# Optimization experiments

Hardware: AMD Instinct MI355X
Metric: run time of the kernel (lower is better)

Reference implementation:

```python
import jax, jax.numpy as jnp
import numpy as np

V, E, H = 32000, 512, 1024  # vocab, embed_dim, hidden_dim
B, S = 32, 64
PAD = 0


def _init(key, shape, fan_in):
    return jax.random.normal(key, shape, jnp.float32) * (1.0 / np.sqrt(fan_in))


def setup_inputs() -> dict:
    key = jax.random.key(0)
    ks = jax.random.split(key, 16)
    tok_embed = _init(ks[0], (V, E), E).at[PAD].set(0.0)  # padding_idx row zeroed
    inp = {
        "image_emb": jax.random.normal(ks[1], (B, E), jnp.float32),
        "retrieved_emb": jax.random.normal(ks[2], (B, E), jnp.float32),
        "tokens_in": jax.random.randint(ks[3], (B, S), 0, V, jnp.int64),
        "tok_embed": tok_embed,
        "init_h_W": _init(ks[4], (H, E), E),
        "init_h_b": jnp.zeros((H,), jnp.float32),
        "gru_W_ih": _init(ks[5], (3 * H, 2 * E), 2 * E),
        "gru_W_hh": _init(ks[6], (3 * H, H), H),
        "gru_b_ih": jnp.zeros((3 * H,), jnp.float32),
        "gru_b_hh": jnp.zeros((3 * H,), jnp.float32),
        "gate_W": _init(ks[7], (1, H + 2 * E), H + 2 * E),
        "gate_b": jnp.zeros((1,), jnp.float32),
        "out_W": _init(ks[8], (V, H), H),
        "out_b": jnp.zeros((V,), jnp.float32),
    }
    return inp


def _gru_cell(x, h, W_ih, W_hh, b_ih, b_hh):
    # PyTorch GRU cell math
    gi = x @ W_ih.T + b_ih  # [B, 3H]
    gh = h @ W_hh.T + b_hh
    i_r, i_z, i_n = jnp.split(gi, 3, axis=-1)
    h_r, h_z, h_n = jnp.split(gh, 3, axis=-1)
    r = jax.nn.sigmoid(i_r + h_r)
    z = jax.nn.sigmoid(i_z + h_z)
    n = jnp.tanh(i_n + r * h_n)
    return (1.0 - z) * n + z * h


def reference(image_emb, retrieved_emb, tokens_in, tok_embed, init_h_W, init_h_b,
              gru_W_ih, gru_W_hh, gru_b_ih, gru_b_hh, gate_W, gate_b, out_W, out_b):
    tok = tok_embed[tokens_in]  # [B, S, E]
    h0 = jnp.tanh(image_emb @ init_h_W.T + init_h_b)  # [B, H]

    def step(h, x_t):
        gate_in = jnp.concatenate([h, image_emb, retrieved_emb], axis=-1)  # [B, H+2E]
        alpha = jax.nn.sigmoid(gate_in @ gate_W.T + gate_b)  # [B, 1]
        fused = alpha * image_emb + (1.0 - alpha) * retrieved_emb  # [B, E]
        gru_in = jnp.concatenate([x_t, fused], axis=-1)  # [B, 2E]
        h_new = _gru_cell(gru_in, h, gru_W_ih, gru_W_hh, gru_b_ih, gru_b_hh)
        logit = h_new @ out_W.T + out_b  # [B, V]
        return h_new, logit

    _, logits = jax.lax.scan(step, h0, jnp.swapaxes(tok, 0, 1))  # [S, B, V]
    return jnp.swapaxes(logits, 0, 1)  # [B, S, V]
```

## Files before the change

### kernel.cpp

```cpp
#include <hip/hip_runtime.h>
#include <hip/hip_bf16.h>
#include <stdint.h>

#define B_ 32
#define S_ 64
#define E_ 512
#define H_ 1024
#define V_ 32000
#define H3_ 3072
#define NPROD 64
#define NCONS 192
#define NGRID (NPROD + NCONS)
#define NPANEL 250
#define NBATCH 16
#define NJOBS (NPANEL * NBATCH)

typedef __bf16 bf16x8 __attribute__((ext_vector_type(8)));
typedef float f32x4 __attribute__((ext_vector_type(4)));
typedef unsigned long long u64_t;
using bf16 = __hip_bfloat16;

__device__ __forceinline__ unsigned short f2bf(float f) {
  __hip_bfloat16 h = __float2bfloat16(f);
  return __builtin_bit_cast(unsigned short, h);
}

__device__ __forceinline__ void async16(void* lds, const void* g) {
  __builtin_amdgcn_global_load_lds(
      (const __attribute__((address_space(1))) unsigned int*)g,
      (__attribute__((address_space(3))) unsigned int*)lds, 16, 0, 0);
}

__device__ __forceinline__ void st_u32(unsigned* p, unsigned v) {
  __hip_atomic_store(p, v, __ATOMIC_RELAXED, __HIP_MEMORY_SCOPE_AGENT);
}
__device__ __forceinline__ unsigned ld_u32(const unsigned* p) {
  return __hip_atomic_load(p, __ATOMIC_RELAXED, __HIP_MEMORY_SCOPE_AGENT);
}
__device__ __forceinline__ f32x4 ld16_mall(const void* p) {
  f32x4 r;
  asm volatile("global_load_dwordx4 %0, %1, off sc0 sc1" : "=v"(r) : "v"(p));
  return r;
}

__device__ __forceinline__ int hswz(int b, int ig) {
  return ((((b >> 4) * 32 + (ig >> 5)) * 64) + ((b & 15) + (((ig >> 3) & 3) << 4))) * 8 + (ig & 7);
}


__global__ void cvt_wb(const float* __restrict__ W, ushort* __restrict__ Wb, long n4) {
  long stride = (long)gridDim.x * blockDim.x;
  for (long i = (long)blockIdx.x * blockDim.x + threadIdx.x; i < n4; i += stride) {
    f32x4 v = *(const f32x4*)(W + i * 4);
    ushort4 o;
    o.x = f2bf(v[0]); o.y = f2bf(v[1]); o.z = f2bf(v[2]); o.w = f2bf(v[3]);
    ((ushort4*)Wb)[i] = o;
  }
}

__global__ void cvt_whh(const float* __restrict__ W, bf16* __restrict__ hi,
                        bf16* __restrict__ lo) {
  size_t idx = ((size_t)blockIdx.x * 256 + threadIdx.x) * 4;
  f32x4 v = *(const f32x4*)(W + idx);
#pragma unroll
  for (int j = 0; j < 4; ++j) {
    bf16 h = __float2bfloat16(v[j]);
    hi[idx + j] = h;
    lo[idx + j] = __float2bfloat16(v[j] - __bfloat162float(h));
  }
}

__global__ void gather_tok(const int* __restrict__ toks, const float* __restrict__ emb,
                           bf16* __restrict__ Abf) {
  int m = blockIdx.x;
  int b = m & 31, t = m >> 5;
  int token = toks[b * S_ + t];
  const float* src = emb + (size_t)token * E_;
  bf16* dst = Abf + (size_t)m * E_;
  int k = threadIdx.x * 4;
  f32x4 v = *(const f32x4*)(src + k);
  dst[k + 0] = __float2bfloat16(v[0]);
  dst[k + 1] = __float2bfloat16(v[1]);
  dst[k + 2] = __float2bfloat16(v[2]);
  dst[k + 3] = __float2bfloat16(v[3]);
}

__global__ void cvt_wihx(const float* __restrict__ Wih, bf16* __restrict__ Wx) {
  int j = blockIdx.x;
  int k = threadIdx.x * 4;
  f32x4 v = *(const f32x4*)(Wih + (size_t)j * 1024 + k);
  bf16* d = Wx + (size_t)j * 512 + k;
  d[0] = __float2bfloat16(v[0]);
  d[1] = __float2bfloat16(v[1]);
  d[2] = __float2bfloat16(v[2]);
  d[3] = __float2bfloat16(v[3]);
}

__global__ void h0_kernel(const float* __restrict__ img, const float* __restrict__ W,
                          const float* __restrict__ bias, float* __restrict__ h32,
                          bf16* __restrict__ hbf0) {
  __shared__ float sim[B_][E_ + 1];
  int tid = threadIdx.x;
  for (int i = tid; i < B_ * E_ / 4; i += 256) {
    f32x4 v = ((const f32x4*)img)[i];
    int r = (i * 4) / E_, c = (i * 4) % E_;
    sim[r][c + 0] = v[0]; sim[r][c + 1] = v[1]; sim[r][c + 2] = v[2]; sim[r][c + 3] = v[3];
  }
  __syncthreads();
  int b = tid & 31, il = tid >> 5;
  int i = blockIdx.x * 8 + il;
  const float* wr = W + (size_t)i * E_;
  float acc = 0.f;
  for (int k = 0; k < E_; k += 4) {
    f32x4 w4 = *(const f32x4*)(wr + k);
    acc += w4[0] * sim[b][k] + w4[1] * sim[b][k + 1] + w4[2] * sim[b][k + 2] + w4[3] * sim[b][k + 3];
  }
  float hv = tanhf(acc + bias[i]);
  h32[b * H_ + i] = hv;
  hbf0[hswz(b, i)] = __float2bfloat16(hv);
}

__global__ void uv_kernel(const float* __restrict__ img, const float* __restrict__ retr,
                          const float* __restrict__ Wih, float* __restrict__ u,
                          float* __restrict__ v) {
  int blk = blockIdx.x;
  bool isU = blk < 384;
  const float* src = isU ? img : retr;
  float* dst = isU ? u : v;
  int j0 = (isU ? blk : blk - 384) * 8;
  __shared__ float sim[B_][E_ + 1];
  int tid = threadIdx.x;
  for (int i = tid; i < B_ * E_ / 4; i += 256) {
    f32x4 vv = ((const f32x4*)src)[i];
    int r = (i * 4) / E_, c = (i * 4) % E_;
    sim[r][c + 0] = vv[0]; sim[r][c + 1] = vv[1]; sim[r][c + 2] = vv[2]; sim[r][c + 3] = vv[3];
  }
  __syncthreads();
  int b = tid & 31;
  int j = j0 + (tid >> 5);
  const float* wr = Wih + (size_t)j * 1024 + 512;
  float acc = 0.f;
  for (int k = 0; k < E_; k += 4) {
    f32x4 w4 = *(const f32x4*)(wr + k);
    acc += w4[0] * sim[b][k] + w4[1] * sim[b][k + 1] + w4[2] * sim[b][k + 2] + w4[3] * sim[b][k + 3];
  }
  dst[b * H3_ + j] = acc;
}

__global__ void cgate_kernel(const float* __restrict__ img, const float* __restrict__ retr,
                             const float* __restrict__ gW, const float* __restrict__ gb,
                             float* __restrict__ cg) {
  int b = blockIdx.x, tid = threadIdx.x;
  float acc = 0.f;
  for (int k = tid; k < E_; k += 256)
    acc += img[b * E_ + k] * gW[1024 + k] + retr[b * E_ + k] * gW[1536 + k];
  __shared__ float red[256];
  red[tid] = acc;
  __syncthreads();
  for (int s = 128; s > 0; s >>= 1) {
    if (tid < s) red[tid] += red[tid + s];
    __syncthreads();
  }
  if (tid == 0) cg[b] = red[0] + gb[0];
}

__device__ __forceinline__ void step_sync(unsigned* flags, int bi, unsigned val) {
  __syncthreads();
  if (threadIdx.x == 0) st_u32(flags + bi * 32, val);
  if (threadIdx.x < NPROD) {
    const unsigned* f = flags + threadIdx.x * 32;
    while (ld_u32(f) < val) __builtin_amdgcn_s_sleep(1);
  }
  __syncthreads();
}

__global__ __launch_bounds__(256, 1) void fused_persist(
    const bf16* __restrict__ WhhHi, const bf16* __restrict__ WhhLo,
    const float* __restrict__ gixAll, const float* __restrict__ u,
    const float* __restrict__ v, const float* __restrict__ cg,
    const float* __restrict__ gW, const float* __restrict__ bih,
    const float* __restrict__ bhh, const float* __restrict__ h32init,
    bf16* __restrict__ hbf, unsigned* __restrict__ flags,
    const bf16* __restrict__ Wb, const float* __restrict__ outb,
    float* __restrict__ out) {
  __shared__ __align__(16) char smem[32768];
  int bi = blockIdx.x;
  int tid = threadIdx.x;

  if (bi < NPROD) {
    int w = tid >> 6, l = tid & 63;
    int lr = l & 15, lk8 = (l >> 4) * 8;
    int kbase = w * 256;
    float(*red)[4][2][64][4] = (float(*)[4][2][64][4])smem;

    bf16x8 whi[3][8], wlo[3][8];
#pragma unroll
    for (int g = 0; g < 3; ++g)
#pragma unroll
      for (int ks = 0; ks < 8; ++ks) {
        size_t off = (size_t)(g * H_ + bi * 16 + lr) * H_ + kbase + ks * 32 + lk8;
        whi[g][ks] = *(const bf16x8*)(WhhHi + off);
        wlo[g][ks] = *(const bf16x8*)(WhhLo + off);
      }
    bf16x8 gwf[8];
#pragma unroll
    for (int ks = 0; ks < 8; ++ks) {
      int kk = (w * 8 + ks) * 32 + (l >> 4) * 8;
      f32x4 g0 = *(const f32x4*)(gW + kk);
      f32x4 g1 = *(const f32x4*)(gW + kk + 4);
      bf16x8 gf;
#pragma unroll
      for (int j = 0; j < 4; ++j) {
        gf[j] = __builtin_bit_cast(__bf16, f2bf(g0[j]));
        gf[j + 4] = __builtin_bit_cast(__bf16, f2bf(g1[j]));
      }
      gwf[ks] = gf;
    }

    int bq = tid >> 3;
    int il0 = (tid & 7) * 2;
    float uq[2][3], vq[2][3], biq[2][3], bhq[2][3], hold[2];
    float cgq = cg[bq];
#pragma unroll
    for (int q = 0; q < 2; ++q) {
      int ig = bi * 16 + il0 + q;
#pragma unroll
      for (int g = 0; g < 3; ++g) {
        uq[q][g] = u[bq * H3_ + g * H_ + ig];
        vq[q][g] = v[bq * H3_ + g * H_ + ig];
        biq[q][g] = bih[g * H_ + ig];
        bhq[q][g] = bhh[g * H_ + ig];
      }
      hold[q] = h32init[bq * H_ + ig];
    }
    int btq = bq >> 4, breg = bq & 3, lrow = ((bq & 15) >> 2) * 16;

    for (int t = 0; t < S_; ++t) {
      const char* hb = (const char*)hbf + (size_t)t * 65536;
      bf16x8 hh_all[2][8];
#pragma unroll
      for (int bt = 0; bt < 2; ++bt)
#pragma unroll
        for (int ks = 0; ks < 8; ++ks) {
          int off = ((bt * 32 + w * 8 + ks) * 64 + l) * 16;
          hh_all[bt][ks] = __builtin_bit_cast(bf16x8, ld16_mall(hb + off));
        }
      float gxv[2][3];
      {
        const float* gx = gixAll + ((size_t)t * B_ + bq) * H3_;
#pragma unroll
        for (int q = 0; q < 2; ++q) {
          int ig = bi * 16 + il0 + q;
          gxv[q][0] = gx[ig];
          gxv[q][1] = gx[H_ + ig];
          gxv[q][2] = gx[2 * H_ + ig];
        }
      }
      asm volatile("s_waitcnt vmcnt(0)" ::: "memory");
      __builtin_amdgcn_sched_barrier(0);

      f32x4 acc[4][2] = {};
#pragma unroll
      for (int ks = 0; ks < 8; ++ks) {
#pragma unroll
        for (int bt = 0; bt < 2; ++bt) {
          bf16x8 hh = hh_all[bt][ks];
          acc[0][bt] = __builtin_amdgcn_mfma_f32_16x16x32_bf16(hh, whi[0][ks], acc[0][bt], 0, 0, 0);
          acc[0][bt] = __builtin_amdgcn_mfma_f32_16x16x32_bf16(hh, wlo[0][ks], acc[0][bt], 0, 0, 0);
          acc[1][bt] = __builtin_amdgcn_mfma_f32_16x16x32_bf16(hh, whi[1][ks], acc[1][bt], 0, 0, 0);
          acc[1][bt] = __builtin_amdgcn_mfma_f32_16x16x32_bf16(hh, wlo[1][ks], acc[1][bt], 0, 0, 0);
          acc[2][bt] = __builtin_amdgcn_mfma_f32_16x16x32_bf16(hh, whi[2][ks], acc[2][bt], 0, 0, 0);
          acc[2][bt] = __builtin_amdgcn_mfma_f32_16x16x32_bf16(hh, wlo[2][ks], acc[2][bt], 0, 0, 0);
          acc[3][bt] = __builtin_amdgcn_mfma_f32_16x16x32_bf16(hh, gwf[ks], acc[3][bt], 0, 0, 0);
        }
      }
#pragma unroll
      for (int g = 0; g < 4; ++g)
#pragma unroll
        for (int bt = 0; bt < 2; ++bt)
          *(f32x4*)&red[w][g][bt][l][0] = acc[g][bt];
      __syncthreads();

      int lane0 = lrow + il0;
      float ad = red[0][3][btq][lane0][breg] + red[1][3][btq][lane0][breg] +
                 red[2][3][btq][lane0][breg] + red[3][3][btq][lane0][breg];
      float a = 1.f / (1.f + expf(-(ad + cgq)));
      unsigned short h16[2];
#pragma unroll
      for (int q = 0; q < 2; ++q) {
        int lane = lrow + il0 + q;
        float sr = red[0][0][btq][lane][breg] + red[1][0][btq][lane][breg] +
                   red[2][0][btq][lane][breg] + red[3][0][btq][lane][breg];
        float sz = red[0][1][btq][lane][breg] + red[1][1][btq][lane][breg] +
                   red[2][1][btq][lane][breg] + red[3][1][btq][lane][breg];
        float sn = red[0][2][btq][lane][breg] + red[1][2][btq][lane][breg] +
                   red[2][2][btq][lane][breg] + red[3][2][btq][lane][breg];
        float ir = gxv[q][0] + a * uq[q][0] + (1.f - a) * vq[q][0] + biq[q][0];
        float iz = gxv[q][1] + a * uq[q][1] + (1.f - a) * vq[q][1] + biq[q][1];
        float in_ = gxv[q][2] + a * uq[q][2] + (1.f - a) * vq[q][2] + biq[q][2];
        float r = 1.f / (1.f + expf(-(ir + sr + bhq[q][0])));
        float z = 1.f / (1.f + expf(-(iz + sz + bhq[q][1])));
        float nn = tanhf(in_ + r * (sn + bhq[q][2]));
        float hv = (1.f - z) * nn + z * hold[q];
        hold[q] = hv;
        h16[q] = f2bf(hv);
      }
      {
        unsigned hipack = (unsigned)h16[0] | ((unsigned)h16[1] << 16);
        int off = hswz(bq, bi * 16 + il0);
        unsigned* hi32 = (unsigned*)hbf + (size_t)(t + 1) * 16384;
        st_u32(hi32 + (off >> 1), hipack);
      }
      if (t < S_ - 1) step_sync(flags, bi, t + 1);
    }
    __syncthreads();
    if (tid == 0) st_u32(flags + bi * 32, S_);

  } else {
    int c = bi - NPROD;
    int l = tid & 63, w = tid >> 6;
    int wm = (w >> 1) * 64, wn = (w & 1) * 64;
    int lr = l & 15, lk = (l >> 4) * 8;
    bf16* Bld = (bf16*)smem;
    char* lB0 = smem + w * 1024;
    const char* hb_base = (const char*)hbf;

    for (int j = c; j < NJOBS; j += NCONS) {
      int batch = j / NPANEL;
      int panel = j - batch * NPANEL;
      int s0 = batch * 4 + 1;
      unsigned need = (unsigned)(batch * 4 + 4);
      if (w == 0) {
        const unsigned* f = flags + l * 32;
        while (ld_u32(f) < need) __builtin_amdgcn_s_sleep(16);
      }
      __builtin_amdgcn_sched_barrier(0);
      __builtin_amdgcn_s_barrier();
      __builtin_amdgcn_sched_barrier(0);

      const bf16* gb = Wb + (size_t)(panel * 128 + w * 16 + (l >> 2)) * 1024 + (l & 3) * 8;
      f32x4 acc[4][4] = {};
      bf16x8 afr[2][4];
#pragma unroll
      for (int mi = 0; mi < 4; ++mi) {
        int r16 = (wm >> 4) + mi;
        const char* p = hb_base + (size_t)(s0 + (r16 >> 1)) * 65536 +
                        (((r16 & 1) * 32 + 0) * 64 + l) * 16;
        afr[0][mi] = __builtin_bit_cast(bf16x8, ld16_mall(p));
      }
#pragma unroll
      for (int kt = 0; kt < 32; ++kt) {
        char* lB = lB0 + (kt & 1) * 8192;
        async16(lB, gb);
        async16(lB + 4096, gb + (size_t)64 * 1024);
        gb += 32;
        if (kt < 31) {
#pragma unroll
          for (int mi = 0; mi < 4; ++mi) {
            int r16 = (wm >> 4) + mi;
            const char* p = hb_base + (size_t)(s0 + (r16 >> 1)) * 65536 +
                            (((r16 & 1) * 32 + (kt + 1)) * 64 + l) * 16;
            afr[(kt + 1) & 1][mi] = __builtin_bit_cast(bf16x8, ld16_mall(p));
          }
          asm volatile("s_waitcnt vmcnt(4)" ::: "memory");
        } else {
          asm volatile("s_waitcnt vmcnt(0)" ::: "memory");
        }
        __builtin_amdgcn_sched_barrier(0);
        __builtin_amdgcn_s_barrier();
        __builtin_amdgcn_sched_barrier(0);
        const bf16* Bh = Bld + (kt & 1) * 4096;
        bf16x8 bfv[4];
#pragma unroll
        for (int ni = 0; ni < 4; ++ni)
          bfv[ni] = *(const bf16x8*)&Bh[(wn + ni * 16 + lr) * 32 + lk];
#pragma unroll
        for (int mi = 0; mi < 4; ++mi)
#pragma unroll
          for (int ni = 0; ni < 4; ++ni)
            acc[mi][ni] = __builtin_amdgcn_mfma_f32_16x16x32_bf16(afr[kt & 1][mi], bfv[ni],
                                                                  acc[mi][ni], 0, 0, 0);
      }
      int cr = (l >> 4) * 4, cc = l & 15;
#pragma unroll
      for (int mi = 0; mi < 4; ++mi)
#pragma unroll
        for (int ni = 0; ni < 4; ++ni) {
          int col = panel * 128 + wn + ni * 16 + cc;
          float bv = outb[col];
#pragma unroll
          for (int rr = 0; rr < 4; ++rr) {
            int gr = wm + mi * 16 + cr + rr;
            int t = s0 - 1 + (gr >> 5);
            int b = gr & 31;
            out[(size_t)(b * S_ + t) * V_ + col] = acc[mi][ni][rr] + bv;
          }
        }
    }
  }
}

__global__ __launch_bounds__(256) void gemm_bt(const bf16* __restrict__ A,
                                               const bf16* __restrict__ Bt,
                                               const float* __restrict__ bias,
                                               float* __restrict__ C, int M, int N, int K) {
  __shared__ bf16 Ald[128 * 32];
  __shared__ bf16 Bld[128 * 32];
  int nb = gridDim.x;
  int bid = blockIdx.x;
  int swz = bid;
  if ((nb & 7) == 0) swz = (bid & 7) * (nb >> 3) + (bid >> 3);
  int mtiles = M >> 7;
  int tm = swz % mtiles, tn = swz / mtiles;
  int tid = threadIdx.x;
  int l = tid & 63, w = tid >> 6;

  const bf16* ga = A + (size_t)(tm * 128 + w * 16 + (l >> 2)) * K + (l & 3) * 8;
  const bf16* gb = Bt + (size_t)(tn * 128 + w * 16 + (l >> 2)) * K + (l & 3) * 8;
  char* lA = (char*)Ald + w * 1024;
  char* lB = (char*)Bld + w * 1024;

  f32x4 acc[4][4] = {};
  int wm = (w >> 1) * 64, wn = (w & 1) * 64;
  int lr = l & 15, lk = (l >> 4) * 8;

  for (int kt = 0; kt < K; kt += 32) {
    async16(lA, ga);
    async16(lA + 4096, ga + (size_t)64 * K);
    async16(lB, gb);
    async16(lB + 4096, gb + (size_t)64 * K);
    ga += 32; gb += 32;
    __syncthreads();
    bf16x8 af[4], bfv[4];
#pragma unroll
    for (int mi = 0; mi < 4; ++mi) af[mi] = *(const bf16x8*)&Ald[(wm + mi * 16 + lr) * 32 + lk];
#pragma unroll
    for (int ni = 0; ni < 4; ++ni) bfv[ni] = *(const bf16x8*)&Bld[(wn + ni * 16 + lr) * 32 + lk];
#pragma unroll
    for (int mi = 0; mi < 4; ++mi)
#pragma unroll
      for (int ni = 0; ni < 4; ++ni)
        acc[mi][ni] = __builtin_amdgcn_mfma_f32_16x16x32_bf16(af[mi], bfv[ni], acc[mi][ni], 0, 0, 0);
    __syncthreads();
  }

  int cr = (l >> 4) * 4, cc = l & 15;
#pragma unroll
  for (int mi = 0; mi < 4; ++mi) {
#pragma unroll
    for (int ni = 0; ni < 4; ++ni) {
      int col = tn * 128 + wn + ni * 16 + cc;
      float bv = bias ? bias[col] : 0.f;
#pragma unroll
      for (int rr = 0; rr < 4; ++rr) {
        int row = tm * 128 + wm + mi * 16 + cr + rr;
        C[(size_t)row * N + col] = acc[mi][ni][rr] + bv;
      }
    }
  }
}

extern "C" void kernel_launch(void* const* d_in, const int* in_sizes, int n_in, void* d_out,
                              int out_size, void* d_ws, size_t ws_size, hipStream_t stream) {
  const float* img  = (const float*)d_in[0];
  const float* retr = (const float*)d_in[1];
  const int*   toks = (const int*)d_in[2];
  const float* temb = (const float*)d_in[3];
  const float* ihW  = (const float*)d_in[4];
  const float* ihb  = (const float*)d_in[5];
  const float* Wih  = (const float*)d_in[6];
  const float* Whh  = (const float*)d_in[7];
  const float* bih  = (const float*)d_in[8];
  const float* bhh  = (const float*)d_in[9];
  const float* gW   = (const float*)d_in[10];
  const float* gb   = (const float*)d_in[11];
  const float* outW = (const float*)d_in[12];
  const float* outb = (const float*)d_in[13];
  float* out = (float*)d_out;

  char* ws = (char*)d_ws;
  bf16* Wb     = (bf16*)ws;  ws += (size_t)V_ * H_ * 2;
  float* gix   = (float*)ws; ws += (size_t)S_ * B_ * H3_ * 4;
  bf16* WhhHi  = (bf16*)ws;  ws += (size_t)H3_ * H_ * 2;
  bf16* WhhLo  = (bf16*)ws;  ws += (size_t)H3_ * H_ * 2;
  bf16* Wihx   = (bf16*)ws;  ws += (size_t)H3_ * E_ * 2;
  bf16* Abf    = (bf16*)ws;  ws += (size_t)B_ * S_ * E_ * 2;
  float* u     = (float*)ws; ws += (size_t)B_ * H3_ * 4;
  float* v     = (float*)ws; ws += (size_t)B_ * H3_ * 4;
  float* h32i  = (float*)ws; ws += (size_t)B_ * H_ * 4;
  bf16* hbf    = (bf16*)ws;  ws += (size_t)(S_ + 1) * B_ * H_ * 2;
  float* cg    = (float*)ws; ws += 128;
  unsigned* flags = (unsigned*)ws; ws += NPROD * 32 * 4;

  cvt_wb<<<2048, 256, 0, stream>>>(outW, (ushort*)Wb, (long)V_ * H_ / 4);
  gather_tok<<<B_ * S_, 128, 0, stream>>>(toks, temb, Abf);
  cvt_wihx<<<H3_, 128, 0, stream>>>(Wih, Wihx);
  gemm_bt<<<(B_ * S_ / 128) * (H3_ / 128), 256, 0, stream>>>(Abf, Wihx, nullptr, gix,
                                                             B_ * S_, H3_, E_);
  cvt_whh<<<H3_ * H_ / 1024, 256, 0, stream>>>(Whh, WhhHi, WhhLo);
  h0_kernel<<<H_ / 8, 256, 0, stream>>>(img, ihW, ihb, h32i, hbf);
  uv_kernel<<<768, 256, 0, stream>>>(img, retr, Wih, u, v);
  cgate_kernel<<<B_, 256, 0, stream>>>(img, retr, gW, gb, cg);
  (void)hipMemsetAsync(flags, 0, NPROD * 32 * 4, stream);

  fused_persist<<<NGRID, 256, 0, stream>>>(WhhHi, WhhLo, gix, u, v, cg, gW, bih, bhh, h32i,
                                           hbf, flags, Wb, outb, out);
}
```

Before: 465.1 us.

## Fold out_W bf16 conversion into consumer blocks and fix panel ownership

```diff
diff --git a/kernel.cpp b/kernel.cpp
--- a/kernel.cpp
+++ b/kernel.cpp
@@ -13,7 +13,6 @@
 #define NGRID (NPROD + NCONS)
 #define NPANEL 250
 #define NBATCH 16
-#define NJOBS (NPANEL * NBATCH)
 
 typedef __bf16 bf16x8 __attribute__((ext_vector_type(8)));
 typedef float f32x4 __attribute__((ext_vector_type(4)));
@@ -47,16 +46,6 @@
   return ((((b >> 4) * 32 + (ig >> 5)) * 64) + ((b & 15) + (((ig >> 3) & 3) << 4))) * 8 + (ig & 7);
 }
 
-
-__global__ void cvt_wb(const float* __restrict__ W, ushort* __restrict__ Wb, long n4) {
-  long stride = (long)gridDim.x * blockDim.x;
-  for (long i = (long)blockIdx.x * blockDim.x + threadIdx.x; i < n4; i += stride) {
-    f32x4 v = *(const f32x4*)(W + i * 4);
-    ushort4 o;
-    o.x = f2bf(v[0]); o.y = f2bf(v[1]); o.z = f2bf(v[2]); o.w = f2bf(v[3]);
-    ((ushort4*)Wb)[i] = o;
-  }
-}
 
 __global__ void cvt_whh(const float* __restrict__ W, bf16* __restrict__ hi,
                         bf16* __restrict__ lo) {
@@ -181,8 +170,8 @@
     const float* __restrict__ gW, const float* __restrict__ bih,
     const float* __restrict__ bhh, const float* __restrict__ h32init,
     bf16* __restrict__ hbf, unsigned* __restrict__ flags,
-    const bf16* __restrict__ Wb, const float* __restrict__ outb,
-    float* __restrict__ out) {
+    const float* __restrict__ outW, bf16* __restrict__ Wb,
+    const float* __restrict__ outb, float* __restrict__ out) {
   __shared__ __align__(16) char smem[32768];
   int bi = blockIdx.x;
   int tid = threadIdx.x;
@@ -320,14 +309,22 @@
     int c = bi - NPROD;
     int l = tid & 63, w = tid >> 6;
     int wm = (w >> 1) * 64, wn = (w & 1) * 64;
-    int lr = l & 15, lk = (l >> 4) * 8;
-    bf16* Bld = (bf16*)smem;
-    char* lB0 = smem + w * 1024;
+    int lr = l & 15, kk8 = (l >> 4) * 8;
     const char* hb_base = (const char*)hbf;
 
-    for (int j = c; j < NJOBS; j += NCONS) {
-      int batch = j / NPANEL;
-      int panel = j - batch * NPANEL;
+    for (int p = c; p < NPANEL; p += NCONS) {
+      const float* src = outW + (size_t)p * 128 * 1024;
+      bf16* dst = Wb + (size_t)p * 128 * 1024;
+      for (int i = tid; i < 128 * 1024 / 4; i += 256) {
+        f32x4 v4 = *(const f32x4*)(src + (size_t)i * 4);
+        ushort4 o;
+        o.x = f2bf(v4[0]); o.y = f2bf(v4[1]); o.z = f2bf(v4[2]); o.w = f2bf(v4[3]);
+        ((ushort4*)dst)[i] = o;
+      }
+    }
+    __syncthreads();
+
+    for (int batch = 0; batch < NBATCH; ++batch) {
       int s0 = batch * 4 + 1;
       unsigned need = (unsigned)(batch * 4 + 4);
       if (w == 0) {
@@ -338,64 +335,66 @@
       __builtin_amdgcn_s_barrier();
       __builtin_amdgcn_sched_barrier(0);
 
-      const bf16* gb = Wb + (size_t)(panel * 128 + w * 16 + (l >> 2)) * 1024 + (l & 3) * 8;
-      f32x4 acc[4][4] = {};
-      bf16x8 afr[2][4];
-#pragma unroll
-      for (int mi = 0; mi < 4; ++mi) {
-        int r16 = (wm >> 4) + mi;
-        const char* p = hb_base + (size_t)(s0 + (r16 >> 1)) * 65536 +
-                        (((r16 & 1) * 32 + 0) * 64 + l) * 16;
-        afr[0][mi] = __builtin_bit_cast(bf16x8, ld16_mall(p));
-      }
-#pragma unroll
-      for (int kt = 0; kt < 32; ++kt) {
-        char* lB = lB0 + (kt & 1) * 8192;
-        async16(lB, gb);
-        async16(lB + 4096, gb + (size_t)64 * 1024);
-        gb += 32;
-        if (kt < 31) {
-#pragma unroll
-          for (int mi = 0; mi < 4; ++mi) {
-            int r16 = (wm >> 4) + mi;
-            const char* p = hb_base + (size_t)(s0 + (r16 >> 1)) * 65536 +
-                            (((r16 & 1) * 32 + (kt + 1)) * 64 + l) * 16;
-            afr[(kt + 1) & 1][mi] = __builtin_bit_cast(bf16x8, ld16_mall(p));
+      for (int p = c; p < NPANEL; p += NCONS) {
+        const bf16* gb0 = Wb + (size_t)(p * 128 + w * 16 + lr) * 1024 + kk8;
+        const bf16* gb1 = Wb + (size_t)(p * 128 + 64 + w * 16 + lr) * 1024 + kk8;
+        f32x4 acc[4][4] = {};
+        bf16x8 afr[2][4];
+#pragma unroll
+        for (int mi = 0; mi < 4; ++mi) {
+          int r16 = (wm >> 4) + mi;
+          const char* pa = hb_base + (size_t)(s0 + (r16 >> 1)) * 65536 +
+                           (((r16 & 1) * 32 + 0) * 64 + l) * 16;
+          afr[0][mi] = __builtin_bit_cast(bf16x8, ld16_mall(pa));
+        }
+#pragma unroll
+        for (int kt = 0; kt < 32; ++kt) {
+          char* lB = smem + (kt & 1) * 8192 + w * 1024;
+          async16(lB, gb0 + kt * 32);
+          async16(lB + 4096, gb1 + kt * 32);
+          if (kt < 31) {
+#pragma unroll
+            for (int mi = 0; mi < 4; ++mi) {
+              int r16 = (wm >> 4) + mi;
+              const char* pa = hb_base + (size_t)(s0 + (r16 >> 1)) * 65536 +
+                               (((r16 & 1) * 32 + (kt + 1)) * 64 + l) * 16;
+              afr[(kt + 1) & 1][mi] = __builtin_bit_cast(bf16x8, ld16_mall(pa));
+            }
+            asm volatile("s_waitcnt vmcnt(4)" ::: "memory");
+          } else {
+            asm volatile("s_waitcnt vmcnt(0)" ::: "memory");
           }
-          asm volatile("s_waitcnt vmcnt(4)" ::: "memory");
-        } else {
-          asm volatile("s_waitcnt vmcnt(0)" ::: "memory");
+          __builtin_amdgcn_sched_barrier(0);
+          __builtin_amdgcn_s_barrier();
+          __builtin_amdgcn_sched_barrier(0);
+          const char* Bh = smem + (kt & 1) * 8192;
+          bf16x8 bfv[4];
+#pragma unroll
+          for (int ni = 0; ni < 4; ++ni)
+            bfv[ni] = *(const bf16x8*)(Bh + ((wn >> 4) + ni) * 1024 + l * 16);
+#pragma unroll
+          for (int mi = 0; mi < 4; ++mi)
+#pragma unroll
+            for (int ni = 0; ni < 4; ++ni)
+              acc[mi][ni] = __builtin_amdgcn_mfma_f32_16x16x32_bf16(afr[kt & 1][mi], bfv[ni],
+                                                                    acc[mi][ni], 0, 0, 0);
         }
-        __builtin_amdgcn_sched_barrier(0);
-        __builtin_amdgcn_s_barrier();
-        __builtin_amdgcn_sched_barrier(0);
-        const bf16* Bh = Bld + (kt & 1) * 4096;
-        bf16x8 bfv[4];
-#pragma unroll
-        for (int ni = 0; ni < 4; ++ni)
-          bfv[ni] = *(const bf16x8*)&Bh[(wn + ni * 16 + lr) * 32 + lk];
+        int cr = (l >> 4) * 4, cc = l & 15;
 #pragma unroll
         for (int mi = 0; mi < 4; ++mi)
 #pragma unroll
-          for (int ni = 0; ni < 4; ++ni)
-            acc[mi][ni] = __builtin_amdgcn_mfma_f32_16x16x32_bf16(afr[kt & 1][mi], bfv[ni],
-                                                                  acc[mi][ni], 0, 0, 0);
-      }
-      int cr = (l >> 4) * 4, cc = l & 15;
-#pragma unroll
-      for (int mi = 0; mi < 4; ++mi)
-#pragma unroll
-        for (int ni = 0; ni < 4; ++ni) {
-          int col = panel * 128 + wn + ni * 16 + cc;
-          float bv = outb[col];
-#pragma unroll
-          for (int rr = 0; rr < 4; ++rr) {
-            int gr = wm + mi * 16 + cr + rr;
-            int t = s0 - 1 + (gr >> 5);
-            int b = gr & 31;
-            out[(size_t)(b * S_ + t) * V_ + col] = acc[mi][ni][rr] + bv;
+          for (int ni = 0; ni < 4; ++ni) {
+            int col = p * 128 + wn + ni * 16 + cc;
+            float bv = outb[col];
+#pragma unroll
+            for (int rr = 0; rr < 4; ++rr) {
+              int gr = wm + mi * 16 + cr + rr;
+              int t = s0 - 1 + (gr >> 5);
+              int b = gr & 31;
+              out[(size_t)(b * S_ + t) * V_ + col] = acc[mi][ni][rr] + bv;
+            }
           }
-        }
+      }
     }
   }
 }
@@ -492,7 +491,6 @@
   float* cg    = (float*)ws; ws += 128;
   unsigned* flags = (unsigned*)ws; ws += NPROD * 32 * 4;
 
-  cvt_wb<<<2048, 256, 0, stream>>>(outW, (ushort*)Wb, (long)V_ * H_ / 4);
   gather_tok<<<B_ * S_, 128, 0, stream>>>(toks, temb, Abf);
   cvt_wihx<<<H3_, 128, 0, stream>>>(Wih, Wihx);
   gemm_bt<<<(B_ * S_ / 128) * (H3_ / 128), 256, 0, stream>>>(Abf, Wihx, nullptr, gix,
@@ -504,5 +502,5 @@
   (void)hipMemsetAsync(flags, 0, NPROD * 32 * 4, stream);
 
   fused_persist<<<NGRID, 256, 0, stream>>>(WhhHi, WhhLo, gix, u, v, cg, gW, bih, bhh, h32i,
-                                           hbf, flags, Wb, outb, out);
-}
+                                           hbf, flags, outW, Wb, outb, out);
+}
```

Result: slower. 925.4 us (+99.0%).
